# Optimization experiments

Hardware: AMD Instinct MI355X
Metric: run time of the kernel (lower is better)

## Reference

```python
import jax, jax.numpy as jnp
import numpy as np

B, G, T, C = 32, 4, 512, 256


def setup_inputs() -> dict:
    key = jax.random.key(0)
    k1, k2, k3 = jax.random.split(key, 3)
    x = jax.random.normal(k1, (B, G, T, C), dtype=jnp.float32)
    # learned per-channel params, initialized around the repo defaults 0.3 / 0.1
    w_input = 0.3 * jax.random.uniform(k2, (C,), dtype=jnp.float32) + 0.15
    w_leak = 0.1 * jax.random.uniform(k3, (C,), dtype=jnp.float32) + 0.05
    return {"x": x, "w_input": w_input, "w_leak": w_leak}


def _heaviside(v):
    # theta_forget: step function with zero gradient (matches @tf.custom_gradient)
    return jax.lax.stop_gradient((v >= 0).astype(v.dtype))


def reference(x, w_input, w_leak):
    # x: (B, G, T, C) -> flatten group into batch, scan over time
    b, g, t, c = x.shape
    V_THRESH = 1.0   # V_thresh default
    T_REF = 1.0      # t_refrectory receives self.thresh (=1) positionally
    xr = jnp.transpose(x.reshape(b * g, t, c), (1, 0, 2))  # (T, N, C)

    def step(carry, xt):
        Vm, R = carry
        R = _heaviside(Vm - V_THRESH) * T_REF + _heaviside(R - 1.0) * (R - 1.0)
        Vm = (w_input * xt + (1.0 - w_leak) * Vm) * _heaviside(-R)
        return (Vm, R), Vm

    zeros = jnp.zeros((b * g, c), dtype=x.dtype)
    _, Vs = jax.lax.scan(step, (zeros, zeros), xr)  # Vs: (T, N, C)
    return jnp.transpose(Vs, (1, 0, 2)).reshape(b, g, t, c)
```

## Files before the change

### kernel.cpp

```cpp
#include <hip/hip_runtime.h>


typedef float f32x4 __attribute__((ext_vector_type(4)));

constexpr int T_STEPS = 512;
constexpr int CCH     = 256;
constexpr int NSEQ    = 128;
constexpr int WIN     = 32;
constexpr int NWIN    = T_STEPS / WIN;

__device__ __forceinline__ void window_barrier() {
    __builtin_amdgcn_sched_barrier(0);
    asm volatile("s_waitcnt lgkmcnt(0)" ::: "memory");
    __builtin_amdgcn_s_barrier();
    __builtin_amdgcn_sched_barrier(0);
}

__global__ __launch_bounds__(256, 1) void lif_kernel(
    const float* __restrict__ x,
    const float* __restrict__ w_input,
    const float* __restrict__ w_leak,
    float* __restrict__ out)
{
#pragma clang fp contract(off)
    __shared__ float obuf[2][WIN][CCH];

    const int j  = threadIdx.x;
    const int wv = j >> 6;
    const int l  = j & 63;
    const int n  = blockIdx.x;

    const float w = w_input[j];
    const float a = 1.0f - w_leak[j];

    const float* xp = x + (size_t)n * T_STEPS * CCH + j;
    float* ob = out + (size_t)n * T_STEPS * CCH + 4 * l;

    float buf[WIN];
#pragma unroll
    for (int k = 0; k < WIN; ++k) buf[k] = xp[(size_t)k * CCH];

    float Vm = 0.0f;

    auto do_stores = [&](int p, int tbase) {
#pragma unroll
        for (int s = 0; s < 8; ++s) {
            const int r = s * 4 + wv;
            const f32x4 vv = *(const f32x4*)&obuf[p][r][4 * l];
            *(f32x4*)(ob + (size_t)(tbase + r) * CCH) = vv;
        }
    };

    auto do_window = [&](int p, int t0, bool refill) {
#pragma unroll
        for (int k = 0; k < WIN; ++k) {
            const float xt = buf[k];
            if (refill) buf[k] = xp[(size_t)(t0 + WIN + k) * CCH];
            const float v = (w * xt) + (a * Vm);
            Vm = (Vm - 1.0f >= 0.0f) ? 0.0f : v;
            obuf[p][k][j] = Vm;
        }
    };

    do_window(0, 0, true);
    window_barrier();
    for (int W = 1; W < NWIN - 1; ++W) {
        do_stores((W - 1) & 1, (W - 1) * WIN);
        do_window(W & 1, W * WIN, true);
        window_barrier();
    }
    do_stores((NWIN - 2) & 1, (NWIN - 2) * WIN);
    do_window((NWIN - 1) & 1, (NWIN - 1) * WIN, false);
    window_barrier();
    do_stores((NWIN - 1) & 1, (NWIN - 1) * WIN);
}

extern "C" void kernel_launch(void* const* d_in, const int* in_sizes, int n_in,
                              void* d_out, int out_size, void* d_ws, size_t ws_size,
                              hipStream_t stream) {
    const float* x       = (const float*)d_in[0];
    const float* w_input = (const float*)d_in[1];
    const float* w_leak  = (const float*)d_in[2];
    float* out = (float*)d_out;

    dim3 grid(NSEQ);
    dim3 block(CCH);
    hipLaunchKernelGGL(lif_kernel, grid, block, 0, stream,
                       x, w_input, w_leak, out);
}
```

Baseline: 30.26 us.

## Stream input through triple-buffered LDS via direct global-to-LDS loads

Input tiles now go straight from global memory into a three-slot LDS ring using global_load_lds in 16-byte chunks. Each load is issued two windows ahead and gated by hand-tuned vmcnt waits. Outputs are stored directly as coalesced scalar stores, so the LDS output staging buffer goes away. The window shrinks to 16 timesteps, which frees registers but adds more barriers. The hard-coded vmcnt counts are fragile and must match the exact load and store instruction counts.

```diff
diff --git a/kernel.cpp b/kernel.cpp
--- a/kernel.cpp
+++ b/kernel.cpp
@@ -1,20 +1,13 @@
 #include <hip/hip_runtime.h>
 
-
-typedef float f32x4 __attribute__((ext_vector_type(4)));
 
 constexpr int T_STEPS = 512;
 constexpr int CCH     = 256;
 constexpr int NSEQ    = 128;
-constexpr int WIN     = 32;
+constexpr int WIN     = 16;
 constexpr int NWIN    = T_STEPS / WIN;
 
-__device__ __forceinline__ void window_barrier() {
-    __builtin_amdgcn_sched_barrier(0);
-    asm volatile("s_waitcnt lgkmcnt(0)" ::: "memory");
-    __builtin_amdgcn_s_barrier();
-    __builtin_amdgcn_sched_barrier(0);
-}
+__device__ __forceinline__ void sfence() { __builtin_amdgcn_sched_barrier(0); }
 
 __global__ __launch_bounds__(256, 1) void lif_kernel(
     const float* __restrict__ x,
@@ -23,56 +16,70 @@
     float* __restrict__ out)
 {
 #pragma clang fp contract(off)
-    __shared__ float obuf[2][WIN][CCH];
+    __shared__ float xw[3][WIN * CCH];
 
-    const int j  = threadIdx.x;
-    const int wv = j >> 6;
-    const int l  = j & 63;
-    const int n  = blockIdx.x;
+    const int tid = threadIdx.x;
+    const int n   = blockIdx.x;
 
-    const float w = w_input[j];
-    const float a = 1.0f - w_leak[j];
+    const float w = w_input[tid];
+    const float a = 1.0f - w_leak[tid];
 
-    const float* xp = x + (size_t)n * T_STEPS * CCH + j;
-    float* ob = out + (size_t)n * T_STEPS * CCH + 4 * l;
+    const float* xg = x   + (size_t)n * T_STEPS * CCH;
+    float*       og = out + (size_t)n * T_STEPS * CCH + tid;
 
-    float buf[WIN];
+    auto issue = [&](int Wt) {
+        float* dst0 = &xw[Wt % 3][(tid >> 6) * 256];
+        const float* src0 = xg + (size_t)Wt * (WIN * CCH) + tid * 4;
 #pragma unroll
-    for (int k = 0; k < WIN; ++k) buf[k] = xp[(size_t)k * CCH];
+        for (int i = 0; i < 4; ++i) {
+            __builtin_amdgcn_global_load_lds(
+                (const __attribute__((address_space(1))) void*)(src0 + i * 1024),
+                (__attribute__((address_space(3))) void*)(dst0 + i * 1024),
+                16, 0, 0);
+        }
+        sfence();
+    };
 
     float Vm = 0.0f;
 
-    auto do_stores = [&](int p, int tbase) {
+    auto compute_store = [&](int Wt) {
+        const float* xb = &xw[Wt % 3][0];
+        float ov[WIN];
 #pragma unroll
-        for (int s = 0; s < 8; ++s) {
-            const int r = s * 4 + wv;
-            const f32x4 vv = *(const f32x4*)&obuf[p][r][4 * l];
-            *(f32x4*)(ob + (size_t)(tbase + r) * CCH) = vv;
+        for (int k = 0; k < WIN; ++k) {
+            const float xt = xb[k * CCH + tid];
+            const float v = (w * xt) + (a * Vm);
+            Vm = (Vm - 1.0f >= 0.0f) ? 0.0f : v;
+            ov[k] = Vm;
         }
+        sfence();
+#pragma unroll
+        for (int k = 0; k < WIN; ++k)
+            og[(size_t)(Wt * WIN + k) * CCH] = ov[k];
+        sfence();
     };
 
-    auto do_window = [&](int p, int t0, bool refill) {
-#pragma unroll
-        for (int k = 0; k < WIN; ++k) {
-            const float xt = buf[k];
-            if (refill) buf[k] = xp[(size_t)(t0 + WIN + k) * CCH];
-            const float v = (w * xt) + (a * Vm);
-            Vm = (Vm - 1.0f >= 0.0f) ? 0.0f : v;
-            obuf[p][k][j] = Vm;
-        }
-    };
+    issue(0); issue(1);
+    asm volatile("s_waitcnt vmcnt(4)" ::: "memory");
+    __builtin_amdgcn_s_barrier();
 
-    do_window(0, 0, true);
-    window_barrier();
-    for (int W = 1; W < NWIN - 1; ++W) {
-        do_stores((W - 1) & 1, (W - 1) * WIN);
-        do_window(W & 1, W * WIN, true);
-        window_barrier();
+    issue(2);
+    compute_store(0);
+    asm volatile("s_waitcnt vmcnt(20)" ::: "memory");
+    __builtin_amdgcn_s_barrier();
+
+    for (int W = 1; W <= 29; ++W) {
+        issue(W + 2);
+        compute_store(W);
+        asm volatile("s_waitcnt vmcnt(36)" ::: "memory");
+        __builtin_amdgcn_s_barrier();
     }
-    do_stores((NWIN - 2) & 1, (NWIN - 2) * WIN);
-    do_window((NWIN - 1) & 1, (NWIN - 1) * WIN, false);
-    window_barrier();
-    do_stores((NWIN - 1) & 1, (NWIN - 1) * WIN);
+
+    compute_store(30);
+    asm volatile("s_waitcnt vmcnt(32)" ::: "memory");
+    __builtin_amdgcn_s_barrier();
+
+    compute_store(31);
 }
 
 extern "C" void kernel_launch(void* const* d_in, const int* in_sizes, int n_in,
```

After: 28.07 us. 7.3% less time.
